# Kernel optimization log

Hardware: AMD Instinct MI355X
Metric: run time of the kernel (lower is better)

Reference implementation:

```python
import jax, jax.numpy as jnp
import numpy as np

HEADS = 4
DIM_HEAD = 64


def setup_inputs() -> dict:
    key = jax.random.key(0)
    k1, k2, k3, k4 = jax.random.split(key, 4)
    dim = 256
    hidden = HEADS * DIM_HEAD  # 256
    x = jax.random.normal(k1, (16, dim, 64, 64), dtype=jnp.float32)
    # 1x1 conv weights stored as [out_c, in_c]
    w_qkv = jax.random.normal(k2, (3 * hidden, dim), dtype=jnp.float32) * (1.0 / np.sqrt(dim))
    w_out = jax.random.normal(k3, (dim, hidden), dtype=jnp.float32) * (1.0 / np.sqrt(hidden))
    b_out = jax.random.normal(k4, (dim,), dtype=jnp.float32) * 0.01
    gamma = jnp.ones((dim,), dtype=jnp.float32) * 1e-05
    return {"x": x, "w_qkv": w_qkv, "w_out": w_out, "b_out": b_out, "gamma": gamma}


def reference(x, w_qkv, w_out, b_out, gamma):
    b, c, h, w = x.shape
    n = h * w
    # 1x1 conv == channel matmul
    qkv = jnp.einsum('oc,bchw->bohw', w_qkv, x)  # [b, 3*heads*dh, h, w]
    qkv = qkv.reshape(b, 3, HEADS, DIM_HEAD, n)  # channel split order: (qkv, heads, c)
    q, k, v = qkv[:, 0], qkv[:, 1], qkv[:, 2]    # each [b, heads, dh, n]
    k = jax.nn.softmax(k, axis=-1)               # softmax over spatial tokens
    context = jnp.einsum('bhdn,bhen->bhde', k, v)  # [b, heads, dh, dh]
    out = jnp.einsum('bhde,bhdn->bhen', context, q)  # [b, heads, dh, n]
    out = out.reshape(b, HEADS * DIM_HEAD, h, w)
    y = jnp.einsum('oc,bchw->bohw', w_out, out) + b_out[None, :, None, None]
    return y * gamma[None, :, None, None] + x
```

## Files before the change

kernel.cpp:

```cpp
#include <hip/hip_runtime.h>
#include <stdint.h>

typedef short s16x8 __attribute__((ext_vector_type(8)));
typedef float f32x4 __attribute__((ext_vector_type(4)));
typedef unsigned int u32x2 __attribute__((ext_vector_type(2)));

typedef const __attribute__((address_space(1))) void glb_cv;
typedef __attribute__((address_space(3))) void lds_v;

__device__ __forceinline__ float bits2f(unsigned short u) {
    union { unsigned int i; float f; } c; c.i = ((unsigned int)u) << 16; return c.f;
}
__device__ __forceinline__ unsigned short f2bits(float f) {
    union { float f; unsigned int i; } c; c.f = f;
    unsigned int x = c.i;
    unsigned int r = (x + 0x7FFFu + ((x >> 16) & 1u)) >> 16;
    return (unsigned short)r;
}
__device__ __forceinline__ unsigned int pack2(float a, float b) {
    return (unsigned int)f2bits(a) | ((unsigned int)f2bits(b) << 16);
}

__device__ __forceinline__ void gl_lds16(const void* g, void* l) {
    __builtin_amdgcn_global_load_lds((glb_cv*)g, (lds_v*)l, 16, 0, 0);
}

__global__ __launch_bounds__(256) void k_cvt(
    const float* __restrict__ src, unsigned short* __restrict__ dst, int n8)
{
    int i = blockIdx.x * 256 + threadIdx.x;
    if (i >= n8) return;
    const float* s = src + (size_t)i * 8;
    float4 a = *(const float4*)s, b = *(const float4*)(s + 4);
    unsigned int q[4] = { pack2(a.x, a.y), pack2(a.z, a.w), pack2(b.x, b.y), pack2(b.z, b.w) };
    *(s16x8*)(dst + (size_t)i * 8) = *(s16x8*)q;
}

__global__ __launch_bounds__(256) void k_transpose(
    const unsigned short* __restrict__ src, unsigned short* __restrict__ dst,
    int RS, int DS)
{
    int dr = blockIdx.x * 256 + threadIdx.x;
    int c0 = blockIdx.y * 8;
    __align__(16) unsigned short tmp[8];
#pragma unroll
    for (int j = 0; j < 8; ++j) tmp[j] = src[(size_t)(c0 + j) * RS + dr];
    *(s16x8*)(dst + (size_t)dr * DS + c0) = *(s16x8*)tmp;
}

__global__ __launch_bounds__(256) void k_prepw(
    const float* __restrict__ wqkv, const float* __restrict__ wout,
    unsigned short* __restrict__ wb, unsigned short* __restrict__ wob,
    unsigned short* __restrict__ WqT)
{
    int i = blockIdx.x * 256 + threadIdx.x;
    if (i < 32768) {
        const float* s; unsigned short* d; int j;
        if (i < 24576) { s = wqkv; d = wb; j = i; }
        else           { s = wout; d = wob; j = i - 24576; }
        const float* sp = s + (size_t)j * 8;
        float4 a = *(const float4*)sp, b = *(const float4*)(sp + 4);
        unsigned int q[4] = { pack2(a.x, a.y), pack2(a.z, a.w), pack2(b.x, b.y), pack2(b.z, b.w) };
        *(s16x8*)(d + (size_t)j * 8) = *(s16x8*)q;
    } else {
        int j = i - 32768;
        int dr = j & 255, c0 = (j >> 8) * 8;
        __align__(16) unsigned short tmp[8];
#pragma unroll
        for (int jj = 0; jj < 8; ++jj)
            tmp[jj] = f2bits(wqkv[(size_t)(c0 + jj) * 256 + dr]);
        *(s16x8*)(WqT + (size_t)dr * 256 + c0) = *(s16x8*)tmp;
    }
}

__global__ __launch_bounds__(256) void k_prep(
    const float* __restrict__ x, unsigned short* __restrict__ xT,
    unsigned short* __restrict__ xbf)
{
    __shared__ unsigned short Ts[64][264];
    int b = blockIdx.y, n0 = blockIdx.x * 64, t = threadIdx.x;
    const float* xb = x + (size_t)b * 1048576;
    unsigned short* xbfb = xbf + (size_t)b * 1048576;
#pragma unroll
    for (int i = 0; i < 16; ++i) {
        int idx = t + i * 256;
        int c = idx >> 4, nq = idx & 15;
        float4 v = *(const float4*)(xb + (size_t)c * 4096 + n0 + nq * 4);
        u32x2 q; q[0] = pack2(v.x, v.y); q[1] = pack2(v.z, v.w);
        *(u32x2*)(xbfb + (size_t)c * 4096 + n0 + nq * 4) = q;
        float vv[4] = { v.x, v.y, v.z, v.w };
#pragma unroll
        for (int e = 0; e < 4; ++e) {
            int ee = (e + c) & 3;
            Ts[nq * 4 + ee][c] = f2bits(vv[ee]);
        }
    }
    __syncthreads();
    unsigned short* xTb = xT + (size_t)b * 1048576 + (size_t)n0 * 256;
#pragma unroll
    for (int i = 0; i < 8; ++i) {
        int idx = t + i * 256;
        int nl = idx >> 5, cg = (idx & 31) * 8;
        *(s16x8*)(xTb + (size_t)nl * 256 + cg) = *(const s16x8*)&Ts[nl][cg];
    }
}

template <int EPI>
__global__ __launch_bounds__(256, 4) void gemm_bt2(
    const unsigned short* __restrict__ A, const unsigned short* __restrict__ Bt,
    void* __restrict__ C,
    int K, int Kstep, int lda, int ldb, int ldc,
    long Abs, long Bbs, long Cbs,
    const float* __restrict__ Xres,
    const float* __restrict__ gamma,
    const float* __restrict__ bias)
{
    __shared__ __align__(16) unsigned short As[2][128 * 32];
    __shared__ __align__(16) unsigned short Bs[2][128 * 32];
    int bz = blockIdx.z;
    int b = bz & 15, kc = bz >> 4;
    int m0 = blockIdx.y * 128, n0 = blockIdx.x * 128;
    const unsigned short* Ab = A + (size_t)b * Abs + (size_t)m0 * lda + (size_t)kc * Kstep;
    const unsigned short* Bb = Bt + (size_t)b * Bbs + (size_t)n0 * ldb + (size_t)kc * Kstep;
    int t = threadIdx.x;
    int w = t >> 6, l = t & 63, lm = l & 15, lq = l >> 4;
    int mw = (w >> 1) * 64, nw = (w & 1) * 64;

    f32x4 acc[4][4];
    f32x4 zero = {0.f, 0.f, 0.f, 0.f};
#pragma unroll
    for (int i = 0; i < 4; ++i)
#pragma unroll
        for (int j = 0; j < 4; ++j) acc[i][j] = zero;

    auto stage = [&](int buf, int kk) {
#pragma unroll
        for (int i = 0; i < 2; ++i) {
            int idx = t + i * 256;
            int r = idx >> 2;
            int sch = (idx & 3) ^ (r & 3);
            int lbase = (i * 256 + w * 64) * 8;
            gl_lds16(Ab + (size_t)r * lda + kk + sch * 8, &As[buf][lbase]);
            gl_lds16(Bb + (size_t)r * ldb + kk + sch * 8, &Bs[buf][lbase]);
        }
    };
    auto compute = [&](int buf) {
        s16x8 af[4], bfr[4];
#pragma unroll
        for (int mi = 0; mi < 4; ++mi) {
            int row = mw + mi * 16 + lm;
            af[mi] = *(const s16x8*)&As[buf][row * 32 + ((lq ^ (row & 3)) << 3)];
        }
#pragma unroll
        for (int ni = 0; ni < 4; ++ni) {
            int row = nw + ni * 16 + lm;
            bfr[ni] = *(const s16x8*)&Bs[buf][row * 32 + ((lq ^ (row & 3)) << 3)];
        }
#pragma unroll
        for (int mi = 0; mi < 4; ++mi)
#pragma unroll
            for (int ni = 0; ni < 4; ++ni)
                acc[mi][ni] = __builtin_amdgcn_mfma_f32_16x16x32_bf16(af[mi], bfr[ni], acc[mi][ni], 0, 0, 0);
    };

    stage(0, 0);
    asm volatile("s_waitcnt vmcnt(0)" ::: "memory");
    __builtin_amdgcn_s_barrier();
    __builtin_amdgcn_sched_barrier(0);

    int cur = 0;
    for (int kk = 32; kk < K; kk += 32) {
        stage(cur ^ 1, kk);
        compute(cur);
        asm volatile("s_waitcnt vmcnt(0)" ::: "memory");
        __builtin_amdgcn_s_barrier();
        __builtin_amdgcn_sched_barrier(0);
        cur ^= 1;
    }
    compute(cur);

    if (EPI == 0) {
        unsigned short* Cb = (unsigned short*)C + (size_t)bz * Cbs;
#pragma unroll
        for (int mi = 0; mi < 4; ++mi)
#pragma unroll
            for (int r = 0; r < 4; ++r) {
                int m = m0 + mw + mi * 16 + lq * 4 + r;
#pragma unroll
                for (int ni = 0; ni < 4; ++ni) {
                    int n = n0 + nw + ni * 16 + lm;
                    Cb[(size_t)m * ldc + n] = f2bits(acc[mi][ni][r]);
                }
            }
    } else {
        float* Cb = (float*)C + (size_t)bz * Cbs;
        const float* Xb = Xres + (size_t)bz * Cbs;
#pragma unroll
        for (int mi = 0; mi < 4; ++mi)
#pragma unroll
            for (int r = 0; r < 4; ++r) {
                int m = m0 + mw + mi * 16 + lq * 4 + r;
                float g = gamma[m], bo = bias[m];
#pragma unroll
                for (int ni = 0; ni < 4; ++ni) {
                    int n = n0 + nw + ni * 16 + lm;
                    size_t idx = (size_t)m * ldc + n;
                    Cb[idx] = g * (acc[mi][ni][r] + bo) + Xb[idx];
                }
            }
    }
}

__global__ __launch_bounds__(256) void gemm64(
    const unsigned short* __restrict__ A, const unsigned short* __restrict__ Bt,
    unsigned short* __restrict__ C,
    int K, int Kstep, int lda, int ldb, int ldc,
    long Abs, long Bbs, long Cbs)
{
    __shared__ __align__(16) unsigned short As[2][64 * 64];
    __shared__ __align__(16) unsigned short Bs[2][64 * 64];
    int bz = blockIdx.z;
    int b = bz & 15, kc = bz >> 4;
    int m0 = blockIdx.y * 64, n0 = blockIdx.x * 64;
    const unsigned short* Ab = A + (size_t)b * Abs + (size_t)m0 * lda + (size_t)kc * Kstep;
    const unsigned short* Bb = Bt + (size_t)b * Bbs + (size_t)n0 * ldb + (size_t)kc * Kstep;
    int t = threadIdx.x;
    int w = t >> 6, l = t & 63, lm = l & 15, lq = l >> 4;
    int mw = (w >> 1) * 32, nw = (w & 1) * 32;

    f32x4 acc[2][2];
    f32x4 zero = {0.f, 0.f, 0.f, 0.f};
#pragma unroll
    for (int i = 0; i < 2; ++i)
#pragma unroll
        for (int j = 0; j < 2; ++j) acc[i][j] = zero;

    auto stage = [&](int buf, int kk) {
#pragma unroll
        for (int i = 0; i < 2; ++i) {
            int idx = t + i * 256;
            int r = idx >> 3;
            int sch = (idx & 7) ^ (r & 7);
            int lbase = (i * 256 + w * 64) * 8;
            gl_lds16(Ab + (size_t)r * lda + kk + sch * 8, &As[buf][lbase]);
            gl_lds16(Bb + (size_t)r * ldb + kk + sch * 8, &Bs[buf][lbase]);
        }
    };
    auto compute = [&](int buf) {
#pragma unroll
        for (int ks = 0; ks < 2; ++ks) {
            s16x8 af[2], bfr[2];
#pragma unroll
            for (int mi = 0; mi < 2; ++mi) {
                int row = mw + mi * 16 + lm;
                af[mi] = *(const s16x8*)&As[buf][row * 64 + (((ks * 4 + lq) ^ (row & 7)) << 3)];
            }
#pragma unroll
            for (int ni = 0; ni < 2; ++ni) {
                int row = nw + ni * 16 + lm;
                bfr[ni] = *(const s16x8*)&Bs[buf][row * 64 + (((ks * 4 + lq) ^ (row & 7)) << 3)];
            }
#pragma unroll
            for (int mi = 0; mi < 2; ++mi)
#pragma unroll
                for (int ni = 0; ni < 2; ++ni)
                    acc[mi][ni] = __builtin_amdgcn_mfma_f32_16x16x32_bf16(af[mi], bfr[ni], acc[mi][ni], 0, 0, 0);
        }
    };

    stage(0, 0);
    asm volatile("s_waitcnt vmcnt(0)" ::: "memory");
    __builtin_amdgcn_s_barrier();
    __builtin_amdgcn_sched_barrier(0);

    int cur = 0;
    for (int kk = 64; kk < K; kk += 64) {
        stage(cur ^ 1, kk);
        compute(cur);
        asm volatile("s_waitcnt vmcnt(0)" ::: "memory");
        __builtin_amdgcn_s_barrier();
        __builtin_amdgcn_sched_barrier(0);
        cur ^= 1;
    }
    compute(cur);

    unsigned short* Cb = C + (size_t)bz * Cbs;
#pragma unroll
    for (int mi = 0; mi < 2; ++mi)
#pragma unroll
        for (int r = 0; r < 4; ++r) {
            int m = m0 + mw + mi * 16 + lq * 4 + r;
#pragma unroll
            for (int ni = 0; ni < 2; ++ni) {
                int n = n0 + nw + ni * 16 + lm;
                Cb[(size_t)m * ldc + n] = f2bits(acc[mi][ni][r]);
            }
        }
}

template <int BF32, int EPI>
__global__ __launch_bounds__(256) void gemm_bt(
    const unsigned short* __restrict__ A, const void* __restrict__ Bt,
    void* __restrict__ C,
    int K, int Kstep, int lda, int ldb, int ldc,
    long Abs, long Bbs, long Cbs,
    const float* __restrict__ Xres,
    const float* __restrict__ gamma,
    const float* __restrict__ bias)
{
    __shared__ unsigned short As[128][72];
    __shared__ unsigned short Bs[128][72];
    int bz = blockIdx.z;
    int b = bz & 15, kc = bz >> 4;
    int m0 = blockIdx.y * 128, n0 = blockIdx.x * 128;
    const unsigned short* Ab = A + (size_t)b * Abs + (size_t)m0 * lda + (size_t)kc * Kstep;
    size_t boff = (size_t)b * Bbs + (size_t)n0 * ldb + (size_t)kc * Kstep;
    int t = threadIdx.x;
    int w = t >> 6, l = t & 63, lm = l & 15, lq = l >> 4;
    int mw = (w >> 1) * 64, nw = (w & 1) * 64;

    f32x4 acc[4][4];
    f32x4 zero = {0.f, 0.f, 0.f, 0.f};
#pragma unroll
    for (int i = 0; i < 4; ++i)
#pragma unroll
        for (int j = 0; j < 4; ++j) acc[i][j] = zero;

    for (int kk = 0; kk < K; kk += 64) {
#pragma unroll
        for (int i = 0; i < 4; ++i) {
            int idx = t + i * 256;
            int r = idx >> 3, ch = idx & 7;
            *(s16x8*)&As[r][ch * 8] = *(const s16x8*)(Ab + (size_t)r * lda + kk + ch * 8);
            if (BF32) {
                const float* bp = (const float*)Bt + boff + (size_t)r * ldb + kk + ch * 8;
                float4 v0 = *(const float4*)bp, v1 = *(const float4*)(bp + 4);
                unsigned int q[4] = { pack2(v0.x, v0.y), pack2(v0.z, v0.w),
                                      pack2(v1.x, v1.y), pack2(v1.z, v1.w) };
                *(s16x8*)&Bs[r][ch * 8] = *(s16x8*)q;
            } else {
                const unsigned short* bp = (const unsigned short*)Bt + boff + (size_t)r * ldb + kk + ch * 8;
                *(s16x8*)&Bs[r][ch * 8] = *(const s16x8*)bp;
            }
        }
        __syncthreads();
#pragma unroll
        for (int ks = 0; ks < 2; ++ks) {
            s16x8 af[4], bfr[4];
#pragma unroll
            for (int mi = 0; mi < 4; ++mi) af[mi]  = *(const s16x8*)&As[mw + mi * 16 + lm][ks * 32 + lq * 8];
#pragma unroll
            for (int ni = 0; ni < 4; ++ni) bfr[ni] = *(const s16x8*)&Bs[nw + ni * 16 + lm][ks * 32 + lq * 8];
#pragma unroll
            for (int mi = 0; mi < 4; ++mi)
#pragma unroll
                for (int ni = 0; ni < 4; ++ni)
                    acc[mi][ni] = __builtin_amdgcn_mfma_f32_16x16x32_bf16(af[mi], bfr[ni], acc[mi][ni], 0, 0, 0);
        }
        __syncthreads();
    }

    if (EPI == 0) {
        unsigned short* Cb = (unsigned short*)C + (size_t)bz * Cbs;
#pragma unroll
        for (int mi = 0; mi < 4; ++mi)
#pragma unroll
            for (int r = 0; r < 4; ++r) {
                int m = m0 + mw + mi * 16 + lq * 4 + r;
#pragma unroll
                for (int ni = 0; ni < 4; ++ni) {
                    int n = n0 + nw + ni * 16 + lm;
                    Cb[(size_t)m * ldc + n] = f2bits(acc[mi][ni][r]);
                }
            }
    } else {
        float* Cb = (float*)C + (size_t)bz * Cbs;
        const float* Xb = Xres + (size_t)bz * Cbs;
#pragma unroll
        for (int mi = 0; mi < 4; ++mi)
#pragma unroll
            for (int r = 0; r < 4; ++r) {
                int m = m0 + mw + mi * 16 + lq * 4 + r;
                float g = gamma[m], bo = bias[m];
#pragma unroll
                for (int ni = 0; ni < 4; ++ni) {
                    int n = n0 + nw + ni * 16 + lm;
                    size_t idx = (size_t)m * ldc + n;
                    Cb[idx] = g * (acc[mi][ni][r] + bo) + Xb[idx];
                }
            }
    }
}

template <int EPI>
__global__ __launch_bounds__(256) void gemm_bn(
    const unsigned short* __restrict__ A, const float* __restrict__ B,
    void* __restrict__ C,
    int K, int lda, int ldb, int ldc,
    long Abs, long Bbs, long Cbs,
    const float* __restrict__ Xres,
    const float* __restrict__ gamma,
    const float* __restrict__ bias)
{
    __shared__ unsigned short As[128][72];
    __shared__ unsigned short Bs[64][130];
    int bz = blockIdx.z;
    int m0 = blockIdx.y * 128, n0 = blockIdx.x * 128;
    const unsigned short* Ab = A + (size_t)bz * Abs + (size_t)m0 * lda;
    const float* Bb = B + (size_t)bz * Bbs + n0;
    int t = threadIdx.x;
    int w = t >> 6, l = t & 63, lm = l & 15, lq = l >> 4;
    int mw = (w >> 1) * 64, nw = (w & 1) * 64;

    f32x4 acc[4][4];
    f32x4 zero = {0.f, 0.f, 0.f, 0.f};
#pragma unroll
    for (int i = 0; i < 4; ++i)
#pragma unroll
        for (int j = 0; j < 4; ++j) acc[i][j] = zero;

    for (int kk = 0; kk < K; kk += 64) {
#pragma unroll
        for (int i = 0; i < 4; ++i) {
            int idx = t + i * 256;
            int r = idx >> 3, ch = idx & 7;
            *(s16x8*)&As[r][ch * 8] = *(const s16x8*)(Ab + (size_t)r * lda + kk + ch * 8);
        }
#pragma unroll
        for (int i = 0; i < 4; ++i) {
            int idx = t + i * 256;
            int c = idx >> 4, cc = idx & 15;
            const float* bp = Bb + (size_t)(kk + c) * ldb + cc * 8;
            float4 v0 = *(const float4*)bp, v1 = *(const float4*)(bp + 4);
            unsigned int* q = (unsigned int*)&Bs[c][cc * 8];
            q[0] = pack2(v0.x, v0.y); q[1] = pack2(v0.z, v0.w);
            q[2] = pack2(v1.x, v1.y); q[3] = pack2(v1.z, v1.w);
        }
        __syncthreads();
#pragma unroll
        for (int ks = 0; ks < 2; ++ks) {
            s16x8 af[4];
#pragma unroll
            for (int mi = 0; mi < 4; ++mi) af[mi] = *(const s16x8*)&As[mw + mi * 16 + lm][ks * 32 + lq * 8];
#pragma unroll
            for (int ni = 0; ni < 4; ++ni) {
                s16x8 bfr;
#pragma unroll
                for (int j = 0; j < 8; ++j) bfr[j] = (short)Bs[ks * 32 + lq * 8 + j][nw + ni * 16 + lm];
#pragma unroll
                for (int mi = 0; mi < 4; ++mi)
                    acc[mi][ni] = __builtin_amdgcn_mfma_f32_16x16x32_bf16(af[mi], bfr, acc[mi][ni], 0, 0, 0);
            }
        }
        __syncthreads();
    }

#pragma unroll
    for (int mi = 0; mi < 4; ++mi)
#pragma unroll
        for (int r = 0; r < 4; ++r) {
            int m = m0 + mw + mi * 16 + lq * 4 + r;
            float g = 0.f, bo = 0.f;
            if (EPI == 1) { g = gamma[m]; bo = bias[m]; }
#pragma unroll
            for (int ni = 0; ni < 4; ++ni) {
                int n = n0 + nw + ni * 16 + lm;
                size_t idx = (size_t)m * ldc + n;
                float v = acc[mi][ni][r];
                if (EPI == 1) {
                    float* Cb = (float*)C + (size_t)bz * Cbs;
                    Cb[idx] = g * (v + bo) + Xres[(size_t)bz * Cbs + idx];
                } else {
                    unsigned short* Cb = (unsigned short*)C + (size_t)bz * Cbs;
                    Cb[idx] = f2bits(v);
                }
            }
        }
}

__global__ __launch_bounds__(256) void k_softmax(unsigned short* __restrict__ kbuf)
{
    unsigned short* p = kbuf + (size_t)blockIdx.x * 4096;
    int t = threadIdx.x;
    __shared__ float red[4];

    s16x8 r0 = *(const s16x8*)(p + t * 16);
    s16x8 r1 = *(const s16x8*)(p + t * 16 + 8);
    float v[16];
    float m = -1e30f;
#pragma unroll
    for (int i = 0; i < 8; ++i) { v[i] = bits2f((unsigned short)r0[i]); v[8 + i] = bits2f((unsigned short)r1[i]); }
#pragma unroll
    for (int i = 0; i < 16; ++i) m = fmaxf(m, v[i]);
#pragma unroll
    for (int off = 32; off >= 1; off >>= 1) m = fmaxf(m, __shfl_xor(m, off));
    if ((t & 63) == 0) red[t >> 6] = m;
    __syncthreads();
    m = fmaxf(fmaxf(red[0], red[1]), fmaxf(red[2], red[3]));
    __syncthreads();

    float s = 0.f;
#pragma unroll
    for (int i = 0; i < 16; ++i) { v[i] = __expf(v[i] - m); s += v[i]; }
#pragma unroll
    for (int off = 32; off >= 1; off >>= 1) s += __shfl_xor(s, off);
    if ((t & 63) == 0) red[t >> 6] = s;
    __syncthreads();
    s = red[0] + red[1] + red[2] + red[3];
    float inv = 1.0f / s;

    __align__(16) unsigned short otmp[16];
#pragma unroll
    for (int i = 0; i < 16; ++i) otmp[i] = f2bits(v[i] * inv);
    *(s16x8*)(p + t * 16) = *(s16x8*)(otmp);
    *(s16x8*)(p + t * 16 + 8) = *(s16x8*)(otmp + 8);
}

template <int NC>
__global__ __launch_bounds__(256) void k_gred(
    const unsigned short* __restrict__ Gp, unsigned short* __restrict__ G)
{
    int gid = blockIdx.x * 256 + threadIdx.x;
    int b = gid >> 13;
    size_t i8 = (size_t)(gid & 8191) * 8;
    float s[8] = {0.f, 0.f, 0.f, 0.f, 0.f, 0.f, 0.f, 0.f};
#pragma unroll
    for (int kc = 0; kc < NC; ++kc) {
        s16x8 v = *(const s16x8*)(Gp + (size_t)(kc * 16 + b) * 65536 + i8);
#pragma unroll
        for (int j = 0; j < 8; ++j) s[j] += bits2f((unsigned short)v[j]);
    }
    __align__(16) unsigned short tmp[8];
#pragma unroll
    for (int j = 0; j < 8; ++j) tmp[j] = f2bits(s[j]);
    *(s16x8*)(G + (size_t)b * 65536 + i8) = *(s16x8*)tmp;
}

__global__ __launch_bounds__(256) void k_ctxw2(
    const unsigned short* __restrict__ G, const unsigned short* __restrict__ wb,
    const unsigned short* __restrict__ wob, unsigned short* __restrict__ W2)
{
    __shared__ unsigned short ctxs[64][72];
    int h = blockIdx.x, b = blockIdx.y;
    int t = threadIdx.x, w = t >> 6, l = t & 63, lm = l & 15, lq = l >> 4;
    const unsigned short* Gb = G + (size_t)b * 65536 + (size_t)(h * 64) * 256;
    const unsigned short* Wv = wb + 131072 + (size_t)(h * 64) * 256;
    f32x4 zero = {0.f, 0.f, 0.f, 0.f};

    f32x4 acc[4];
#pragma unroll
    for (int i = 0; i < 4; ++i) acc[i] = zero;
    for (int kk = 0; kk < 256; kk += 32) {
        s16x8 a = *(const s16x8*)(Gb + (size_t)(w * 16 + lm) * 256 + kk + lq * 8);
#pragma unroll
        for (int ni = 0; ni < 4; ++ni) {
            s16x8 bb = *(const s16x8*)(Wv + (size_t)(ni * 16 + lm) * 256 + kk + lq * 8);
            acc[ni] = __builtin_amdgcn_mfma_f32_16x16x32_bf16(a, bb, acc[ni], 0, 0, 0);
        }
    }
#pragma unroll
    for (int ni = 0; ni < 4; ++ni)
#pragma unroll
        for (int r = 0; r < 4; ++r)
            ctxs[w * 16 + lq * 4 + r][ni * 16 + lm] = f2bits(acc[ni][r]);
    __syncthreads();

    f32x4 acc2[4][4];
#pragma unroll
    for (int i = 0; i < 4; ++i)
#pragma unroll
        for (int j = 0; j < 4; ++j) acc2[i][j] = zero;
#pragma unroll
    for (int ks = 0; ks < 2; ++ks) {
        s16x8 af[4], bfr[4];
#pragma unroll
        for (int mi = 0; mi < 4; ++mi)
            af[mi] = *(const s16x8*)(wob + (size_t)(w * 64 + mi * 16 + lm) * 256 + h * 64 + ks * 32 + lq * 8);
#pragma unroll
        for (int ni = 0; ni < 4; ++ni) bfr[ni] = *(const s16x8*)&ctxs[ni * 16 + lm][ks * 32 + lq * 8];
#pragma unroll
        for (int mi = 0; mi < 4; ++mi)
#pragma unroll
            for (int ni = 0; ni < 4; ++ni)
                acc2[mi][ni] = __builtin_amdgcn_mfma_f32_16x16x32_bf16(af[mi], bfr[ni], acc2[mi][ni], 0, 0, 0);
    }
    unsigned short* W2b = W2 + (size_t)b * 65536;
#pragma unroll
    for (int mi = 0; mi < 4; ++mi)
#pragma unroll
        for (int r = 0; r < 4; ++r) {
            int o = w * 64 + mi * 16 + lq * 4 + r;
#pragma unroll
            for (int ni = 0; ni < 4; ++ni)
                W2b[(size_t)o * 256 + h * 64 + ni * 16 + lm] = f2bits(acc2[mi][ni][r]);
        }
}

extern "C" void kernel_launch(void* const* d_in, const int* in_sizes, int n_in,
                              void* d_out, int out_size, void* d_ws, size_t ws_size,
                              hipStream_t stream)
{
    (void)in_sizes; (void)n_in; (void)out_size;
    const float* x      = (const float*)d_in[0];
    const float* w_qkv  = (const float*)d_in[1];
    const float* w_out  = (const float*)d_in[2];
    const float* b_out  = (const float*)d_in[3];
    const float* gamma  = (const float*)d_in[4];

    char* ws = (char*)d_ws;
    const size_t NEED = 40501248;

    if (ws_size >= NEED) {
        unsigned short* xT  = (unsigned short*)ws;
        unsigned short* W3  = (unsigned short*)(ws + 33554432);
        unsigned short* Gp  = (unsigned short*)(ws + 35651584);
        unsigned short* WqT = (unsigned short*)(ws + 39845888);
        unsigned short* wb  = (unsigned short*)(ws + 39976960);
        unsigned short* wob = (unsigned short*)(ws + 40370176);
        unsigned short* kbuf = (unsigned short*)d_out;
        unsigned short* xbf  = (unsigned short*)d_out + 16777216;
        unsigned short* G    = (unsigned short*)d_out;
        unsigned short* W2   = (unsigned short*)d_out + 1048576;

        k_prepw<<<dim3(160), 256, 0, stream>>>(w_qkv, w_out, wb, wob, WqT);

        k_prep<<<dim3(64, 16), 256, 0, stream>>>(x, xT, xbf);

        gemm_bt2<0><<<dim3(32, 2, 16), 256, 0, stream>>>(
            wb + 65536, xT, kbuf, 256, 0, 256, 256, 4096,
            0L, 1048576L, 1048576L, nullptr, nullptr, nullptr);

        k_softmax<<<dim3(4096), 256, 0, stream>>>(kbuf);

        gemm64<<<dim3(4, 4, 32), 256, 0, stream>>>(
            kbuf, xbf, Gp, 2048, 2048, 4096, 4096, 256,
            1048576L, 1048576L, 65536L);

        k_gred<2><<<dim3(512), 256, 0, stream>>>(Gp, G);

        k_ctxw2<<<dim3(4, 16), 256, 0, stream>>>(G, wb, wob, W2);

        gemm64<<<dim3(4, 4, 16), 256, 0, stream>>>(
            W2, WqT, W3, 256, 0, 256, 256, 256,
            65536L, 0L, 65536L);

        gemm_bt2<1><<<dim3(32, 2, 16), 256, 0, stream>>>(
            W3, xT, d_out, 256, 0, 256, 256, 4096,
            65536L, 1048576L, 1048576L, x, gamma, b_out);
    } else {
        unsigned short* kbuf = (unsigned short*)d_out;
        unsigned short* Gp  = (unsigned short*)(ws);
        unsigned short* G   = (unsigned short*)(ws + 16777216);
        unsigned short* W2  = (unsigned short*)(ws + 18874368);
        unsigned short* W3  = (unsigned short*)(ws + 20971520);
        unsigned short* WqT = (unsigned short*)(ws + 23068672);
        unsigned short* wb  = (unsigned short*)(ws + 23199744);
        unsigned short* wob = (unsigned short*)(ws + 23592960);

        k_cvt<<<dim3(96), 256, 0, stream>>>(w_qkv, wb, 24576);
        k_cvt<<<dim3(32), 256, 0, stream>>>(w_out, wob, 8192);
        k_transpose<<<dim3(1, 32, 1), 256, 0, stream>>>(wb, WqT, 256, 256);

        gemm_bn<0><<<dim3(32, 2, 16), 256, 0, stream>>>(
            wb + 65536, x, kbuf, 256, 256, 4096, 4096,
            0L, 1048576L, 1048576L, nullptr, nullptr, nullptr);

        k_softmax<<<dim3(4096), 256, 0, stream>>>(kbuf);

        gemm_bt<1, 0><<<dim3(2, 2, 128), 256, 0, stream>>>(
            kbuf, x, Gp, 512, 512, 4096, 4096, 256,
            1048576L, 1048576L, 65536L, nullptr, nullptr, nullptr);

        k_gred<8><<<dim3(512), 256, 0, stream>>>(Gp, G);
        k_ctxw2<<<dim3(4, 16), 256, 0, stream>>>(G, wb, wob, W2);

        gemm_bt<0, 0><<<dim3(2, 2, 16), 256, 0, stream>>>(
            W2, WqT, W3, 256, 0, 256, 256, 256,
            65536L, 0L, 65536L, nullptr, nullptr, nullptr);

        gemm_bn<1><<<dim3(32, 2, 16), 256, 0, stream>>>(
            W3, x, d_out, 256, 256, 4096, 4096,
            65536L, 1048576L, 1048576L, x, gamma, b_out);
    }
}
```

Baseline: 228.9 us.

## Triple-buffer GEMM pipelines, merge prep kernels, fold split-K reduction into ctx kernel

Both GEMM kernels move from double to triple LDS buffering with a depth-2 prefetch and a partial vmcnt wait, so global loads overlap more with MFMA compute. Occupancy hints drop to 3 blocks per CU to fit the larger LDS footprint. The weight-prep kernel is merged into the x-prep launch as an extra grid row, removing one launch. The split-K partial Gram reduction kernel is removed by having the context kernel accumulate both K-chunk partials directly, which removes a launch and a round trip through memory but adds a little redundant load work per block.

```diff
diff --git a/kernel.cpp b/kernel.cpp
--- a/kernel.cpp
+++ b/kernel.cpp
@@ -48,37 +48,42 @@
     *(s16x8*)(dst + (size_t)dr * DS + c0) = *(s16x8*)tmp;
 }
 
-__global__ __launch_bounds__(256) void k_prepw(
+__global__ __launch_bounds__(256) void k_prep(
+    const float* __restrict__ x, unsigned short* __restrict__ xT,
+    unsigned short* __restrict__ xbf,
     const float* __restrict__ wqkv, const float* __restrict__ wout,
     unsigned short* __restrict__ wb, unsigned short* __restrict__ wob,
     unsigned short* __restrict__ WqT)
 {
-    int i = blockIdx.x * 256 + threadIdx.x;
-    if (i < 32768) {
-        const float* s; unsigned short* d; int j;
-        if (i < 24576) { s = wqkv; d = wb; j = i; }
-        else           { s = wout; d = wob; j = i - 24576; }
-        const float* sp = s + (size_t)j * 8;
-        float4 a = *(const float4*)sp, b = *(const float4*)(sp + 4);
-        unsigned int q[4] = { pack2(a.x, a.y), pack2(a.z, a.w), pack2(b.x, b.y), pack2(b.z, b.w) };
-        *(s16x8*)(d + (size_t)j * 8) = *(s16x8*)q;
-    } else {
-        int j = i - 32768;
-        int dr = j & 255, c0 = (j >> 8) * 8;
-        __align__(16) unsigned short tmp[8];
-#pragma unroll
-        for (int jj = 0; jj < 8; ++jj)
-            tmp[jj] = f2bits(wqkv[(size_t)(c0 + jj) * 256 + dr]);
-        *(s16x8*)(WqT + (size_t)dr * 256 + c0) = *(s16x8*)tmp;
-    }
-}
-
-__global__ __launch_bounds__(256) void k_prep(
-    const float* __restrict__ x, unsigned short* __restrict__ xT,
-    unsigned short* __restrict__ xbf)
-{
+    int t = threadIdx.x;
+    if (blockIdx.y == 16) {
+#pragma unroll
+        for (int it = 0; it < 3; ++it) {
+            int i = blockIdx.x * 256 + t + it * 16384;
+            if (i >= 40960) break;
+            if (i < 32768) {
+                const float* s; unsigned short* d; int j;
+                if (i < 24576) { s = wqkv; d = wb; j = i; }
+                else           { s = wout; d = wob; j = i - 24576; }
+                const float* sp = s + (size_t)j * 8;
+                float4 a = *(const float4*)sp, b2 = *(const float4*)(sp + 4);
+                unsigned int q[4] = { pack2(a.x, a.y), pack2(a.z, a.w),
+                                      pack2(b2.x, b2.y), pack2(b2.z, b2.w) };
+                *(s16x8*)(d + (size_t)j * 8) = *(s16x8*)q;
+            } else {
+                int j = i - 32768;
+                int dr = j & 255, c0 = (j >> 8) * 8;
+                __align__(16) unsigned short tmp[8];
+#pragma unroll
+                for (int jj = 0; jj < 8; ++jj)
+                    tmp[jj] = f2bits(wqkv[(size_t)(c0 + jj) * 256 + dr]);
+                *(s16x8*)(WqT + (size_t)dr * 256 + c0) = *(s16x8*)tmp;
+            }
+        }
+        return;
+    }
     __shared__ unsigned short Ts[64][264];
-    int b = blockIdx.y, n0 = blockIdx.x * 64, t = threadIdx.x;
+    int b = blockIdx.y, n0 = blockIdx.x * 64;
     const float* xb = x + (size_t)b * 1048576;
     unsigned short* xbfb = xbf + (size_t)b * 1048576;
 #pragma unroll
@@ -106,7 +111,7 @@
 }
 
 template <int EPI>
-__global__ __launch_bounds__(256, 4) void gemm_bt2(
+__global__ __launch_bounds__(256, 3) void gemm_bt2(
     const unsigned short* __restrict__ A, const unsigned short* __restrict__ Bt,
     void* __restrict__ C,
     int K, int Kstep, int lda, int ldb, int ldc,
@@ -115,8 +120,8 @@
     const float* __restrict__ gamma,
     const float* __restrict__ bias)
 {
-    __shared__ __align__(16) unsigned short As[2][128 * 32];
-    __shared__ __align__(16) unsigned short Bs[2][128 * 32];
+    __shared__ __align__(16) unsigned short As[3][128 * 32];
+    __shared__ __align__(16) unsigned short Bs[3][128 * 32];
     int bz = blockIdx.z;
     int b = bz & 15, kc = bz >> 4;
     int m0 = blockIdx.y * 128, n0 = blockIdx.x * 128;
@@ -163,21 +168,33 @@
                 acc[mi][ni] = __builtin_amdgcn_mfma_f32_16x16x32_bf16(af[mi], bfr[ni], acc[mi][ni], 0, 0, 0);
     };
 
+    const int NT = K >> 5;
     stage(0, 0);
-    asm volatile("s_waitcnt vmcnt(0)" ::: "memory");
+    if (NT > 1) {
+        stage(1, 32);
+        asm volatile("s_waitcnt vmcnt(4)" ::: "memory");
+    } else {
+        asm volatile("s_waitcnt vmcnt(0)" ::: "memory");
+    }
     __builtin_amdgcn_s_barrier();
     __builtin_amdgcn_sched_barrier(0);
 
-    int cur = 0;
-    for (int kk = 32; kk < K; kk += 32) {
-        stage(cur ^ 1, kk);
-        compute(cur);
-        asm volatile("s_waitcnt vmcnt(0)" ::: "memory");
-        __builtin_amdgcn_s_barrier();
-        __builtin_amdgcn_sched_barrier(0);
-        cur ^= 1;
-    }
-    compute(cur);
+    int bc = 0;
+    for (int tt = 0; tt < NT; ++tt) {
+        compute(bc);
+        if (tt + 2 < NT) {
+            int bs = bc + 2; if (bs >= 3) bs -= 3;
+            stage(bs, (tt + 2) << 5);
+            asm volatile("s_waitcnt vmcnt(4)" ::: "memory");
+            __builtin_amdgcn_s_barrier();
+            __builtin_amdgcn_sched_barrier(0);
+        } else if (tt + 1 < NT) {
+            asm volatile("s_waitcnt vmcnt(0)" ::: "memory");
+            __builtin_amdgcn_s_barrier();
+            __builtin_amdgcn_sched_barrier(0);
+        }
+        if (++bc == 3) bc = 0;
+    }
 
     if (EPI == 0) {
         unsigned short* Cb = (unsigned short*)C + (size_t)bz * Cbs;
@@ -211,14 +228,14 @@
     }
 }
 
-__global__ __launch_bounds__(256) void gemm64(
+__global__ __launch_bounds__(256, 3) void gemm64(
     const unsigned short* __restrict__ A, const unsigned short* __restrict__ Bt,
     unsigned short* __restrict__ C,
     int K, int Kstep, int lda, int ldb, int ldc,
     long Abs, long Bbs, long Cbs)
 {
-    __shared__ __align__(16) unsigned short As[2][64 * 64];
-    __shared__ __align__(16) unsigned short Bs[2][64 * 64];
+    __shared__ __align__(16) unsigned short As[3][64 * 64];
+    __shared__ __align__(16) unsigned short Bs[3][64 * 64];
     int bz = blockIdx.z;
     int b = bz & 15, kc = bz >> 4;
     int m0 = blockIdx.y * 64, n0 = blockIdx.x * 64;
@@ -268,21 +285,33 @@
         }
     };
 
+    const int NT = K >> 6;
     stage(0, 0);
-    asm volatile("s_waitcnt vmcnt(0)" ::: "memory");
+    if (NT > 1) {
+        stage(1, 64);
+        asm volatile("s_waitcnt vmcnt(4)" ::: "memory");
+    } else {
+        asm volatile("s_waitcnt vmcnt(0)" ::: "memory");
+    }
     __builtin_amdgcn_s_barrier();
     __builtin_amdgcn_sched_barrier(0);
 
-    int cur = 0;
-    for (int kk = 64; kk < K; kk += 64) {
-        stage(cur ^ 1, kk);
-        compute(cur);
-        asm volatile("s_waitcnt vmcnt(0)" ::: "memory");
-        __builtin_amdgcn_s_barrier();
-        __builtin_amdgcn_sched_barrier(0);
-        cur ^= 1;
-    }
-    compute(cur);
+    int bc = 0;
+    for (int tt = 0; tt < NT; ++tt) {
+        compute(bc);
+        if (tt + 2 < NT) {
+            int bs = bc + 2; if (bs >= 3) bs -= 3;
+            stage(bs, (tt + 2) << 6);
+            asm volatile("s_waitcnt vmcnt(4)" ::: "memory");
+            __builtin_amdgcn_s_barrier();
+            __builtin_amdgcn_sched_barrier(0);
+        } else if (tt + 1 < NT) {
+            asm volatile("s_waitcnt vmcnt(0)" ::: "memory");
+            __builtin_amdgcn_s_barrier();
+            __builtin_amdgcn_sched_barrier(0);
+        }
+        if (++bc == 3) bc = 0;
+    }
 
     unsigned short* Cb = C + (size_t)bz * Cbs;
 #pragma unroll
@@ -536,6 +565,69 @@
     *(s16x8*)(G + (size_t)b * 65536 + i8) = *(s16x8*)tmp;
 }
 
+__global__ __launch_bounds__(256) void k_ctxw2g(
+    const unsigned short* __restrict__ Gp, const unsigned short* __restrict__ wb,
+    const unsigned short* __restrict__ wob, unsigned short* __restrict__ W2)
+{
+    __shared__ unsigned short ctxs[64][72];
+    int h = blockIdx.x, b = blockIdx.y;
+    int t = threadIdx.x, w = t >> 6, l = t & 63, lm = l & 15, lq = l >> 4;
+    const unsigned short* Wv = wb + 131072 + (size_t)(h * 64) * 256;
+    f32x4 zero = {0.f, 0.f, 0.f, 0.f};
+
+    f32x4 acc[4];
+#pragma unroll
+    for (int i = 0; i < 4; ++i) acc[i] = zero;
+#pragma unroll
+    for (int kc = 0; kc < 2; ++kc) {
+        const unsigned short* Gb = Gp + (size_t)(kc * 16 + b) * 65536 + (size_t)(h * 64) * 256;
+        for (int kk = 0; kk < 256; kk += 32) {
+            s16x8 a = *(const s16x8*)(Gb + (size_t)(w * 16 + lm) * 256 + kk + lq * 8);
+#pragma unroll
+            for (int ni = 0; ni < 4; ++ni) {
+                s16x8 bb = *(const s16x8*)(Wv + (size_t)(ni * 16 + lm) * 256 + kk + lq * 8);
+                acc[ni] = __builtin_amdgcn_mfma_f32_16x16x32_bf16(a, bb, acc[ni], 0, 0, 0);
+            }
+        }
+    }
+#pragma unroll
+    for (int ni = 0; ni < 4; ++ni)
+#pragma unroll
+        for (int r = 0; r < 4; ++r)
+            ctxs[w * 16 + lq * 4 + r][ni * 16 + lm] = f2bits(acc[ni][r]);
+    __syncthreads();
+
+    f32x4 acc2[4][4];
+#pragma unroll
+    for (int i = 0; i < 4; ++i)
+#pragma unroll
+        for (int j = 0; j < 4; ++j) acc2[i][j] = zero;
+#pragma unroll
+    for (int ks = 0; ks < 2; ++ks) {
+        s16x8 af[4], bfr[4];
+#pragma unroll
+        for (int mi = 0; mi < 4; ++mi)
+            af[mi] = *(const s16x8*)(wob + (size_t)(w * 64 + mi * 16 + lm) * 256 + h * 64 + ks * 32 + lq * 8);
+#pragma unroll
+        for (int ni = 0; ni < 4; ++ni) bfr[ni] = *(const s16x8*)&ctxs[ni * 16 + lm][ks * 32 + lq * 8];
+#pragma unroll
+        for (int mi = 0; mi < 4; ++mi)
+#pragma unroll
+            for (int ni = 0; ni < 4; ++ni)
+                acc2[mi][ni] = __builtin_amdgcn_mfma_f32_16x16x32_bf16(af[mi], bfr[ni], acc2[mi][ni], 0, 0, 0);
+    }
+    unsigned short* W2b = W2 + (size_t)b * 65536;
+#pragma unroll
+    for (int mi = 0; mi < 4; ++mi)
+#pragma unroll
+        for (int r = 0; r < 4; ++r) {
+            int o = w * 64 + mi * 16 + lq * 4 + r;
+#pragma unroll
+            for (int ni = 0; ni < 4; ++ni)
+                W2b[(size_t)o * 256 + h * 64 + ni * 16 + lm] = f2bits(acc2[mi][ni][r]);
+        }
+}
+
 __global__ __launch_bounds__(256) void k_ctxw2(
     const unsigned short* __restrict__ G, const unsigned short* __restrict__ wb,
     const unsigned short* __restrict__ wob, unsigned short* __restrict__ W2)
@@ -619,12 +711,9 @@
         unsigned short* wob = (unsigned short*)(ws + 40370176);
         unsigned short* kbuf = (unsigned short*)d_out;
         unsigned short* xbf  = (unsigned short*)d_out + 16777216;
-        unsigned short* G    = (unsigned short*)d_out;
         unsigned short* W2   = (unsigned short*)d_out + 1048576;
 
-        k_prepw<<<dim3(160), 256, 0, stream>>>(w_qkv, w_out, wb, wob, WqT);
-
-        k_prep<<<dim3(64, 16), 256, 0, stream>>>(x, xT, xbf);
+        k_prep<<<dim3(64, 17), 256, 0, stream>>>(x, xT, xbf, w_qkv, w_out, wb, wob, WqT);
 
         gemm_bt2<0><<<dim3(32, 2, 16), 256, 0, stream>>>(
             wb + 65536, xT, kbuf, 256, 0, 256, 256, 4096,
@@ -636,9 +725,7 @@
             kbuf, xbf, Gp, 2048, 2048, 4096, 4096, 256,
             1048576L, 1048576L, 65536L);
 
-        k_gred<2><<<dim3(512), 256, 0, stream>>>(Gp, G);
-
-        k_ctxw2<<<dim3(4, 16), 256, 0, stream>>>(G, wb, wob, W2);
+        k_ctxw2g<<<dim3(4, 16), 256, 0, stream>>>(Gp, wb, wob, W2);
 
         gemm64<<<dim3(4, 4, 16), 256, 0, stream>>>(
             W2, WqT, W3, 256, 0, 256, 256, 256,
```

Result: no change. 229.9 us, median of 2 (+0.4%).
